# Kernel tuning notes

Measured on AMD Instinct MI355X. Metric: run time of the kernel, lower is better.

Reference implementation:

```python
import jax, jax.numpy as jnp
import numpy as np

N = 100000
E = 1600000
D_IN = 128
D_HID = 128
D_OUT = 128


def setup_inputs() -> dict:
    key = jax.random.key(0)
    ks = jax.random.split(key, 12)
    x = jax.random.normal(ks[0], (N, D_IN), dtype=jnp.float32)
    edge_index = jax.random.randint(ks[1], (2, E), 0, N, dtype=jnp.int32)
    def lin(k, fan_in, fan_out):
        s = 1.0 / np.sqrt(fan_in)
        return jax.random.uniform(k, (fan_in, fan_out), jnp.float32, -s, s)
    dims = [(D_IN, D_HID), (D_HID, D_HID), (D_HID, D_OUT)]
    inp = {"x": x, "edge_index": edge_index}
    for i, (fi, fo) in enumerate(dims):
        inp[f"Wl{i}"] = lin(ks[2 + 3 * i], fi, fo)
        inp[f"Wr{i}"] = lin(ks[3 + 3 * i], fi, fo)
        inp[f"b{i}"] = jnp.zeros((fo,), jnp.float32)
    return inp


def _sage_conv(h, row, col, Wl, Wr, b):
    # mean aggregation over incoming neighbors: out[i] = mean_{j->i} h[j]
    n = h.shape[0]
    agg = jax.ops.segment_sum(h[col], row, num_segments=n)  # [N, d]
    deg = jax.ops.segment_sum(jnp.ones_like(row, dtype=h.dtype), row, num_segments=n)
    agg = agg / jnp.maximum(deg, 1.0)[:, None]
    return agg @ Wl + b + h @ Wr


def reference(x, edge_index, Wl0, Wr0, b0, Wl1, Wr1, b1, Wl2, Wr2, b2):
    row, col = edge_index[0], edge_index[1]  # dst, src
    h1 = jax.nn.relu(_sage_conv(x, row, col, Wl0, Wr0, b0))   # dropout is no-op in eval
    h2 = jax.nn.relu(_sage_conv(h1, row, col, Wl1, Wr1, b1))
    h3 = jax.nn.relu(_sage_conv(h2, row, col, Wl2, Wr2, b2))
    return (h1, h2, h3)
```

## Files before the change

### kernel.cpp

```cpp
#include <hip/hip_runtime.h>

#define NN 100000
#define NE 1600000
#define DD 128
#define BM 64
#define NPB 256
#define NBUCK 391
#define ECHUNK 8192
#define NBLK_PART 196
#define CAP 8192
#define CVX_BLK 800
#define CVW_BLK 384

typedef __attribute__((ext_vector_type(4))) float f32x4;
typedef __attribute__((ext_vector_type(8))) short bf16x8;

__device__ inline unsigned short f2bf(float f) {
    unsigned int x = __builtin_bit_cast(unsigned int, f);
    unsigned int r = x + 0x7fffu + ((x >> 16) & 1u);
    return (unsigned short)(r >> 16);
}
__device__ inline float bf_lo(unsigned int u) { return __builtin_bit_cast(float, u << 16); }
__device__ inline float bf_hi(unsigned int u) { return __builtin_bit_cast(float, u & 0xffff0000u); }
__device__ inline unsigned int packbf(float a, float b) {
    return (unsigned int)f2bf(a) | ((unsigned int)f2bf(b) << 16);
}

__device__ inline void load_g2l_16(const void* gsrc, void* ldst) {
    __builtin_amdgcn_global_load_lds(
        (const __attribute__((address_space(1))) void*)(uintptr_t)gsrc,
        (__attribute__((address_space(3))) void*)(uintptr_t)ldst,
        16, 0, 0);
}


__global__ __launch_bounds__(256) void prep_kernel(
    const float* __restrict__ x, unsigned short* __restrict__ xb,
    const float* __restrict__ w0, const float* __restrict__ w1,
    const float* __restrict__ w2, const float* __restrict__ w3,
    const float* __restrict__ w4, const float* __restrict__ w5,
    unsigned short* __restrict__ wtall,
    const int* __restrict__ row, int* __restrict__ gcnt) {
    __shared__ int cnt[NBUCK];
    const int b = blockIdx.x;
    if (b < CVX_BLK) {
        int i = b * 256 + threadIdx.x;
        const int n4 = NN * DD / 4;
        for (; i < n4; i += CVX_BLK * 256) {
            float4 v = reinterpret_cast<const float4*>(x)[i];
            ushort4 o;
            o.x = f2bf(v.x); o.y = f2bf(v.y); o.z = f2bf(v.z); o.w = f2bf(v.w);
            reinterpret_cast<ushort4*>(xb)[i] = o;
        }
    } else if (b < CVX_BLK + CVW_BLK) {
        int t = (b - CVX_BLK) * 256 + threadIdx.x;
        int i = t >> 14;
        int r = t & 16383;
        const float* W = (i == 0) ? w0 : (i == 1) ? w1 : (i == 2) ? w2
                        : (i == 3) ? w3 : (i == 4) ? w4 : w5;
        int c = r >> 7, k = r & 127;
        wtall[t] = f2bf(W[k * DD + c]);
    } else {
        for (int i = threadIdx.x; i < NBUCK; i += 256) cnt[i] = 0;
        __syncthreads();
        int base = (b - CVX_BLK - CVW_BLK) * ECHUNK;
        int end = base + ECHUNK; if (end > NE) end = NE;
        for (int i = base + threadIdx.x; i < end; i += 256)
            atomicAdd(&cnt[row[i] >> 8], 1);
        __syncthreads();
        for (int i = threadIdx.x; i < NBUCK; i += 256) {
            int c = cnt[i];
            if (c) atomicAdd(&gcnt[i], c);
        }
    }
}


__global__ __launch_bounds__(512) void bucket_scan(const int* __restrict__ gcnt,
                                                   int* __restrict__ gbase) {
    __shared__ int sm[512];
    int t = threadIdx.x;
    sm[t] = (t < NBUCK) ? gcnt[t] : 0;
    __syncthreads();
    for (int off = 1; off < 512; off <<= 1) {
        int add = (t >= off) ? sm[t - off] : 0;
        __syncthreads();
        sm[t] += add;
        __syncthreads();
    }
    if (t < NBUCK) gbase[t + 1] = sm[t];
    if (t == 0) gbase[0] = 0;
}

__global__ __launch_bounds__(256) void bucket_scatter(const int* __restrict__ row,
                                                      const int* __restrict__ col,
                                                      const int* __restrict__ gbase,
                                                      int* __restrict__ gcursor,
                                                      uint2* __restrict__ ebuf) {
    __shared__ int cnt[NBUCK];
    __shared__ int base[NBUCK];
    for (int i = threadIdx.x; i < NBUCK; i += 256) cnt[i] = 0;
    __syncthreads();
    int cbase = blockIdx.x * ECHUNK;
    int cend = cbase + ECHUNK; if (cend > NE) cend = NE;
    for (int i = cbase + threadIdx.x; i < cend; i += 256)
        atomicAdd(&cnt[row[i] >> 8], 1);
    __syncthreads();
    for (int i = threadIdx.x; i < NBUCK; i += 256) {
        int c = cnt[i];
        cnt[i] = 0;
        base[i] = c ? (gbase[i] + atomicAdd(&gcursor[i], c)) : 0;
    }
    __syncthreads();
    for (int i = cbase + threadIdx.x; i < cend; i += 256) {
        int r = row[i], c = col[i];
        int b = r >> 8;
        int k = atomicAdd(&cnt[b], 1);
        ebuf[base[b] + k] = uint2{(unsigned)r, (unsigned)c};
    }
}

__global__ __launch_bounds__(256) void csr_build(const uint2* __restrict__ ebuf,
                                                 const int* __restrict__ gbase,
                                                 int* __restrict__ offs,
                                                 int* __restrict__ csr_col) {
    __shared__ int dcnt[NPB];
    __shared__ int doff[NPB];
    __shared__ int sm[NPB];
    __shared__ int stage[CAP];
    const int b = blockIdx.x;
    const int es = gbase[b], ee = gbase[b + 1];
    const int m = ee - es;
    const int t = threadIdx.x;
    const int nbase = b * NPB;

    dcnt[t] = 0;
    __syncthreads();
    for (int i = es + t; i < ee; i += 256) {
        int ln = (int)ebuf[i].x - nbase;
        atomicAdd(&dcnt[ln], 1);
    }
    __syncthreads();
    sm[t] = dcnt[t];
    __syncthreads();
    for (int off = 1; off < 256; off <<= 1) {
        int add = (t >= off) ? sm[t - off] : 0;
        __syncthreads();
        sm[t] += add;
        __syncthreads();
    }
    doff[t] = sm[t] - dcnt[t];
    int node = nbase + t;
    if (node < NN) offs[node + 1] = es + sm[t];
    if (b == 0 && t == 0) offs[0] = 0;
    dcnt[t] = 0;
    __syncthreads();

    if (m <= CAP) {
        for (int i = es + t; i < ee; i += 256) {
            uint2 e = ebuf[i];
            int ln = (int)e.x - nbase;
            int k = atomicAdd(&dcnt[ln], 1);
            stage[doff[ln] + k] = (int)e.y;
        }
        __syncthreads();
        for (int i = t; i < m; i += 256) csr_col[es + i] = stage[i];
    } else {
        for (int i = es + t; i < ee; i += 256) {
            uint2 e = ebuf[i];
            int ln = (int)e.x - nbase;
            int k = atomicAdd(&dcnt[ln], 1);
            csr_col[es + doff[ln] + k] = (int)e.y;
        }
    }
}


__global__ __launch_bounds__(256) void fused_layer(
    const unsigned short* __restrict__ hb,
    const int* __restrict__ offs, const int* __restrict__ csr_col,
    const unsigned short* __restrict__ WlT, const unsigned short* __restrict__ WrT,
    const float* __restrict__ bias, float* __restrict__ out,
    unsigned short* __restrict__ hbn) {
    __shared__ uint4 smem4[2048];
    char* AldsB = (char*)smem4;
    char* HldsB = AldsB + 16384;
    const int row0 = blockIdx.x * BM;
    const int tid = threadIdx.x;
    const int w = tid >> 6, l = tid & 63;

    const char* Hsrc = (const char*)(hb + (size_t)row0 * DD);
#pragma unroll
    for (int j = 0; j < 4; ++j) {
        int base = w * 4096 + j * 1024;
        int doff = base + l * 16;
        int soff = doff ^ (((doff >> 8) & 7) << 4);
        if (row0 + (doff >> 8) < NN) load_g2l_16(Hsrc + soff, HldsB + base);
    }

    const int g16 = tid >> 4, lane = tid & 15;
    for (int i = 0; i < 4; ++i) {
        const int rloc = g16 * 4 + i;
        const int node = row0 + rloc;
        float a0 = 0, a1 = 0, a2 = 0, a3 = 0, a4 = 0, a5 = 0, a6 = 0, a7 = 0;
        float inv = 0.0f;
        if (node < NN) {
            int s = offs[node], e = offs[node + 1];
            int p = s;
            for (; p + 8 <= e; p += 8) {
                uint4 v[8];
#pragma unroll
                for (int q = 0; q < 8; ++q) {
                    int c = csr_col[p + q];
                    v[q] = *reinterpret_cast<const uint4*>(hb + (size_t)c * DD + lane * 8);
                }
#pragma unroll
                for (int q = 0; q < 8; ++q) {
                    a0 += bf_lo(v[q].x); a1 += bf_hi(v[q].x);
                    a2 += bf_lo(v[q].y); a3 += bf_hi(v[q].y);
                    a4 += bf_lo(v[q].z); a5 += bf_hi(v[q].z);
                    a6 += bf_lo(v[q].w); a7 += bf_hi(v[q].w);
                }
            }
            for (; p < e; ++p) {
                int c = csr_col[p];
                uint4 v = *reinterpret_cast<const uint4*>(hb + (size_t)c * DD + lane * 8);
                a0 += bf_lo(v.x); a1 += bf_hi(v.x);
                a2 += bf_lo(v.y); a3 += bf_hi(v.y);
                a4 += bf_lo(v.z); a5 += bf_hi(v.z);
                a6 += bf_lo(v.w); a7 += bf_hi(v.w);
            }
            inv = (e > s) ? (1.0f / (float)(e - s)) : 0.0f;
        }
        uint4 o;
        o.x = packbf(a0 * inv, a1 * inv);
        o.y = packbf(a2 * inv, a3 * inv);
        o.z = packbf(a4 * inv, a5 * inv);
        o.w = packbf(a6 * inv, a7 * inv);
        int off = (rloc << 8) + ((lane * 16) ^ ((rloc & 7) << 4));
        *reinterpret_cast<uint4*>(AldsB + off) = o;
    }
    __syncthreads();

    const int wr = w & 1, wc = w >> 1;
    const int lrow = l & 15, lg = l >> 4;

    f32x4 acc[2][4];
#pragma unroll
    for (int m = 0; m < 2; ++m)
#pragma unroll
        for (int n = 0; n < 4; ++n) acc[m][n] = (f32x4){0.f, 0.f, 0.f, 0.f};

    float bv[4];
#pragma unroll
    for (int n = 0; n < 4; ++n) bv[n] = bias[wc * 64 + n * 16 + lrow];

#pragma unroll
    for (int kb = 0; kb < 4; ++kb) {
        const int kbyte = kb * 64 + lg * 16;
        bf16x8 aA[2], aH[2];
#pragma unroll
        for (int m = 0; m < 2; ++m) {
            int rloc = wr * 32 + m * 16 + lrow;
            int off = (rloc << 8) + kbyte;
            off ^= (rloc & 7) << 4;
            aA[m] = *reinterpret_cast<const bf16x8*>(AldsB + off);
            aH[m] = *reinterpret_cast<const bf16x8*>(HldsB + off);
        }
        bf16x8 bL[4], bR[4];
#pragma unroll
        for (int n = 0; n < 4; ++n) {
            size_t woff = ((size_t)(wc * 64 + n * 16 + lrow) << 7) + kb * 32 + lg * 8;
            bL[n] = *reinterpret_cast<const bf16x8*>(WlT + woff);
            bR[n] = *reinterpret_cast<const bf16x8*>(WrT + woff);
        }
#pragma unroll
        for (int m = 0; m < 2; ++m)
#pragma unroll
            for (int n = 0; n < 4; ++n) {
                acc[m][n] = __builtin_amdgcn_mfma_f32_16x16x32_bf16(aA[m], bL[n], acc[m][n], 0, 0, 0);
                acc[m][n] = __builtin_amdgcn_mfma_f32_16x16x32_bf16(aH[m], bR[n], acc[m][n], 0, 0, 0);
            }
    }

    __syncthreads();
    float* otile = (float*)smem4;
#pragma unroll
    for (int m = 0; m < 2; ++m) {
        int rb = wr * 32 + m * 16 + lg * 4;
#pragma unroll
        for (int n = 0; n < 4; ++n) {
            int c = wc * 64 + n * 16 + lrow;
#pragma unroll
            for (int j = 0; j < 4; ++j)
                otile[(rb + j) * DD + c] = fmaxf(acc[m][n][j] + bv[n], 0.0f);
        }
    }
    __syncthreads();
    const f32x4* t4 = (const f32x4*)smem4;
#pragma unroll
    for (int it = 0; it < 8; ++it) {
        int idx = it * 256 + tid;
        int r = idx >> 5;
        int gr = row0 + r;
        if (gr < NN) {
            f32x4 v = t4[idx];
            __builtin_nontemporal_store(v, (f32x4*)out + (size_t)gr * 32 + (idx & 31));
            if (hbn) {
                uint2 pk;
                pk.x = packbf(v[0], v[1]);
                pk.y = packbf(v[2], v[3]);
                *((uint2*)hbn + (size_t)gr * 32 + (idx & 31)) = pk;
            }
        }
    }
}

extern "C" void kernel_launch(void* const* d_in, const int* in_sizes, int n_in,
                              void* d_out, int out_size, void* d_ws, size_t ws_size,
                              hipStream_t stream) {
    const float* x = (const float*)d_in[0];
    const int* ei = (const int*)d_in[1];
    const int* row = ei;
    const int* col = ei + NE;
    const float* Wl[3] = {(const float*)d_in[2], (const float*)d_in[5], (const float*)d_in[8]};
    const float* Wr[3] = {(const float*)d_in[3], (const float*)d_in[6], (const float*)d_in[9]};
    const float* bb[3] = {(const float*)d_in[4], (const float*)d_in[7], (const float*)d_in[10]};
    float* out = (float*)d_out;

    char* ws = (char*)d_ws;
    auto carve = [&](size_t bytes) {
        char* p = ws;
        ws += (bytes + 255) & ~(size_t)255;
        return p;
    };
    unsigned short* buf0 = (unsigned short*)carve((size_t)NN * DD * 2);
    unsigned short* buf1 = (unsigned short*)carve((size_t)NN * DD * 2);
    unsigned short* wtall = (unsigned short*)carve((size_t)6 * DD * DD * 2);
    int* gcnt    = (int*)carve((size_t)2 * NBUCK * sizeof(int));
    int* gcursor = gcnt + NBUCK;
    int* gbase   = (int*)carve((size_t)(NBUCK + 1) * sizeof(int));
    int* offs    = (int*)carve((size_t)(NN + 1) * sizeof(int));
    uint2* ebuf  = (uint2*)carve((size_t)NE * sizeof(uint2));
    int* csr_col = (int*)carve((size_t)NE * sizeof(int));

    hipMemsetAsync(gcnt, 0, (size_t)2 * NBUCK * sizeof(int), stream);

    prep_kernel<<<CVX_BLK + CVW_BLK + NBLK_PART, 256, 0, stream>>>(
        x, buf0, Wl[0], Wr[0], Wl[1], Wr[1], Wl[2], Wr[2], wtall, row, gcnt);
    bucket_scan<<<1, 512, 0, stream>>>(gcnt, gbase);
    bucket_scatter<<<NBLK_PART, 256, 0, stream>>>(row, col, gbase, gcursor, ebuf);
    csr_build<<<NBUCK, 256, 0, stream>>>(ebuf, gbase, offs, csr_col);

    const int ngrid = (NN + BM - 1) / BM;

    unsigned short* hin = buf0;
    unsigned short* hout = buf1;
    for (int lyr = 0; lyr < 3; ++lyr) {
        float* o = out + (size_t)lyr * NN * DD;
        fused_layer<<<ngrid, 256, 0, stream>>>(
            hin, offs, csr_col,
            wtall + (size_t)2 * lyr * DD * DD, wtall + (size_t)(2 * lyr + 1) * DD * DD,
            bb[lyr], o, (lyr < 2) ? hout : (unsigned short*)nullptr);
        unsigned short* t = hin; hin = hout; hout = t;
    }
}
```

Before: 350.5 us.

## Split layer into feature-sliced gather kernel and separate GEMM kernel

Stores node features in eight 16-feature column slices (32 bytes per node per slice) so each aggregation block gathers from one 3.2MB slice that can stay resident in cache. The layer is split into an aggregation kernel, which uses dynamic row stealing via an LDS atomic counter and writes a sliced aggregate buffer, and a GEMM kernel that loads the sliced aggregate and self tiles with a new swizzle. The input conversion becomes its own kernel that writes the sliced layout. In exchange it adds an extra round trip of the aggregate buffer through global memory and an extra kernel launch per layer.

```diff
diff --git a/kernel.cpp b/kernel.cpp
--- a/kernel.cpp
+++ b/kernel.cpp
@@ -9,9 +9,12 @@
 #define ECHUNK 8192
 #define NBLK_PART 196
 #define CAP 8192
-#define CVX_BLK 800
 #define CVW_BLK 384
-
+#define SLICE_SHORTS ((size_t)NN * 16)
+#define AGG_TILE 1024
+#define AGG_GRID ((98) * 8)
+
+typedef __attribute__((ext_vector_type(2))) float f32x2;
 typedef __attribute__((ext_vector_type(4))) float f32x4;
 typedef __attribute__((ext_vector_type(8))) short bf16x8;
 
@@ -34,8 +37,7 @@
 }
 
 
-__global__ __launch_bounds__(256) void prep_kernel(
-    const float* __restrict__ x, unsigned short* __restrict__ xb,
+__global__ __launch_bounds__(256) void prep_wh(
     const float* __restrict__ w0, const float* __restrict__ w1,
     const float* __restrict__ w2, const float* __restrict__ w3,
     const float* __restrict__ w4, const float* __restrict__ w5,
@@ -43,17 +45,8 @@
     const int* __restrict__ row, int* __restrict__ gcnt) {
     __shared__ int cnt[NBUCK];
     const int b = blockIdx.x;
-    if (b < CVX_BLK) {
-        int i = b * 256 + threadIdx.x;
-        const int n4 = NN * DD / 4;
-        for (; i < n4; i += CVX_BLK * 256) {
-            float4 v = reinterpret_cast<const float4*>(x)[i];
-            ushort4 o;
-            o.x = f2bf(v.x); o.y = f2bf(v.y); o.z = f2bf(v.z); o.w = f2bf(v.w);
-            reinterpret_cast<ushort4*>(xb)[i] = o;
-        }
-    } else if (b < CVX_BLK + CVW_BLK) {
-        int t = (b - CVX_BLK) * 256 + threadIdx.x;
+    if (b < CVW_BLK) {
+        int t = b * 256 + threadIdx.x;
         int i = t >> 14;
         int r = t & 16383;
         const float* W = (i == 0) ? w0 : (i == 1) ? w1 : (i == 2) ? w2
@@ -63,7 +56,7 @@
     } else {
         for (int i = threadIdx.x; i < NBUCK; i += 256) cnt[i] = 0;
         __syncthreads();
-        int base = (b - CVX_BLK - CVW_BLK) * ECHUNK;
+        int base = (b - CVW_BLK) * ECHUNK;
         int end = base + ECHUNK; if (end > NE) end = NE;
         for (int i = base + threadIdx.x; i < end; i += 256)
             atomicAdd(&cnt[row[i] >> 8], 1);
@@ -71,6 +64,38 @@
         for (int i = threadIdx.x; i < NBUCK; i += 256) {
             int c = cnt[i];
             if (c) atomicAdd(&gcnt[i], c);
+        }
+    }
+}
+
+__global__ __launch_bounds__(256) void conv_x_sliced(const float* __restrict__ x,
+                                                     unsigned short* __restrict__ xs) {
+    __shared__ unsigned short tile[BM * DD];
+    const int row0 = blockIdx.x * BM;
+    const int tid = threadIdx.x;
+    char* ldsB = (char*)tile;
+#pragma unroll
+    for (int it = 0; it < 8; ++it) {
+        int idx = it * 256 + tid;
+        int r = idx >> 5, q4 = idx & 31;
+        if (row0 + r < NN) {
+            float4 v = *reinterpret_cast<const float4*>(&x[(size_t)(row0 + r) * DD + q4 * 4]);
+            uint2 pk;
+            pk.x = packbf(v.x, v.y);
+            pk.y = packbf(v.z, v.w);
+            *reinterpret_cast<uint2*>(ldsB + r * 256 + q4 * 8) = pk;
+        }
+    }
+    __syncthreads();
+#pragma unroll
+    for (int it = 0; it < 4; ++it) {
+        int u = it * 256 + tid;
+        int f = u >> 7, rem = u & 127;
+        int r = rem >> 1, half = rem & 1;
+        int n = row0 + r;
+        if (n < NN) {
+            uint4 v = *reinterpret_cast<const uint4*>(ldsB + r * 256 + f * 32 + half * 16);
+            *reinterpret_cast<uint4*>(xs + (size_t)f * SLICE_SHORTS + (size_t)n * 16 + half * 8) = v;
         }
     }
 }
@@ -176,69 +201,88 @@
 }
 
 
-__global__ __launch_bounds__(256) void fused_layer(
-    const unsigned short* __restrict__ hb,
-    const int* __restrict__ offs, const int* __restrict__ csr_col,
+__global__ __launch_bounds__(512) void agg_sliced(const unsigned short* __restrict__ hs,
+                                                  const int* __restrict__ offs,
+                                                  const int* __restrict__ csr_col,
+                                                  unsigned short* __restrict__ aggs) {
+    __shared__ int nextrow;
+    if (threadIdx.x == 0) nextrow = 0;
+    __syncthreads();
+    const int f = blockIdx.x & 7;
+    const int node0 = (blockIdx.x >> 3) * AGG_TILE;
+    const int lane = threadIdx.x & 63;
+    const int half = threadIdx.x & 1;
+    const unsigned short* hsf = hs + (size_t)f * SLICE_SHORTS + half * 8;
+    unsigned short* aggf = aggs + (size_t)f * SLICE_SHORTS + half * 8;
+
+    while (true) {
+        int r = 0;
+        if (!(lane & 1)) r = atomicAdd(&nextrow, 1);
+        r = __shfl(r, lane & ~1, 64);
+        if (r >= AGG_TILE) break;
+        int n = node0 + r;
+        if (n >= NN) continue;
+        int s = offs[n], e = offs[n + 1];
+        f32x2 a0 = {0.f, 0.f}, a1 = {0.f, 0.f}, a2 = {0.f, 0.f}, a3 = {0.f, 0.f};
+        int p = s;
+        for (; p + 8 <= e; p += 8) {
+            uint4 v[8];
+#pragma unroll
+            for (int q = 0; q < 8; ++q) {
+                int c = csr_col[p + q];
+                v[q] = *reinterpret_cast<const uint4*>(hsf + (size_t)c * 16);
+            }
+#pragma unroll
+            for (int q = 0; q < 8; ++q) {
+                a0 += (f32x2){bf_lo(v[q].x), bf_hi(v[q].x)};
+                a1 += (f32x2){bf_lo(v[q].y), bf_hi(v[q].y)};
+                a2 += (f32x2){bf_lo(v[q].z), bf_hi(v[q].z)};
+                a3 += (f32x2){bf_lo(v[q].w), bf_hi(v[q].w)};
+            }
+        }
+        for (; p < e; ++p) {
+            int c = csr_col[p];
+            uint4 v = *reinterpret_cast<const uint4*>(hsf + (size_t)c * 16);
+            a0 += (f32x2){bf_lo(v.x), bf_hi(v.x)};
+            a1 += (f32x2){bf_lo(v.y), bf_hi(v.y)};
+            a2 += (f32x2){bf_lo(v.z), bf_hi(v.z)};
+            a3 += (f32x2){bf_lo(v.w), bf_hi(v.w)};
+        }
+        float inv = (e > s) ? (1.0f / (float)(e - s)) : 0.0f;
+        uint4 o;
+        o.x = packbf(a0[0] * inv, a0[1] * inv);
+        o.y = packbf(a1[0] * inv, a1[1] * inv);
+        o.z = packbf(a2[0] * inv, a2[1] * inv);
+        o.w = packbf(a3[0] * inv, a3[1] * inv);
+        *reinterpret_cast<uint4*>(aggf + (size_t)n * 16) = o;
+    }
+}
+
+
+__global__ __launch_bounds__(256) void gemm_sliced(
+    const unsigned short* __restrict__ aggs, const unsigned short* __restrict__ hs,
     const unsigned short* __restrict__ WlT, const unsigned short* __restrict__ WrT,
     const float* __restrict__ bias, float* __restrict__ out,
     unsigned short* __restrict__ hbn) {
     __shared__ uint4 smem4[2048];
-    char* AldsB = (char*)smem4;
-    char* HldsB = AldsB + 16384;
+    char* ldsB = (char*)smem4;
     const int row0 = blockIdx.x * BM;
     const int tid = threadIdx.x;
     const int w = tid >> 6, l = tid & 63;
 
-    const char* Hsrc = (const char*)(hb + (size_t)row0 * DD);
-#pragma unroll
-    for (int j = 0; j < 4; ++j) {
-        int base = w * 4096 + j * 1024;
-        int doff = base + l * 16;
-        int soff = doff ^ (((doff >> 8) & 7) << 4);
-        if (row0 + (doff >> 8) < NN) load_g2l_16(Hsrc + soff, HldsB + base);
-    }
-
-    const int g16 = tid >> 4, lane = tid & 15;
-    for (int i = 0; i < 4; ++i) {
-        const int rloc = g16 * 4 + i;
-        const int node = row0 + rloc;
-        float a0 = 0, a1 = 0, a2 = 0, a3 = 0, a4 = 0, a5 = 0, a6 = 0, a7 = 0;
-        float inv = 0.0f;
-        if (node < NN) {
-            int s = offs[node], e = offs[node + 1];
-            int p = s;
-            for (; p + 8 <= e; p += 8) {
-                uint4 v[8];
-#pragma unroll
-                for (int q = 0; q < 8; ++q) {
-                    int c = csr_col[p + q];
-                    v[q] = *reinterpret_cast<const uint4*>(hb + (size_t)c * DD + lane * 8);
-                }
-#pragma unroll
-                for (int q = 0; q < 8; ++q) {
-                    a0 += bf_lo(v[q].x); a1 += bf_hi(v[q].x);
-                    a2 += bf_lo(v[q].y); a3 += bf_hi(v[q].y);
-                    a4 += bf_lo(v[q].z); a5 += bf_hi(v[q].z);
-                    a6 += bf_lo(v[q].w); a7 += bf_hi(v[q].w);
-                }
-            }
-            for (; p < e; ++p) {
-                int c = csr_col[p];
-                uint4 v = *reinterpret_cast<const uint4*>(hb + (size_t)c * DD + lane * 8);
-                a0 += bf_lo(v.x); a1 += bf_hi(v.x);
-                a2 += bf_lo(v.y); a3 += bf_hi(v.y);
-                a4 += bf_lo(v.z); a5 += bf_hi(v.z);
-                a6 += bf_lo(v.w); a7 += bf_hi(v.w);
-            }
-            inv = (e > s) ? (1.0f / (float)(e - s)) : 0.0f;
-        }
-        uint4 o;
-        o.x = packbf(a0 * inv, a1 * inv);
-        o.y = packbf(a2 * inv, a3 * inv);
-        o.z = packbf(a4 * inv, a5 * inv);
-        o.w = packbf(a6 * inv, a7 * inv);
-        int off = (rloc << 8) + ((lane * 16) ^ ((rloc & 7) << 4));
-        *reinterpret_cast<uint4*>(AldsB + off) = o;
+#pragma unroll
+    for (int j = 0; j < 8; ++j) {
+        int u = w * 8 + j;
+        int chunk = u >> 1, halfc = u & 1;
+        int tile = chunk >> 3, f = chunk & 7;
+        int pos = halfc * 1024 + l * 16;
+        int r = pos >> 5, sub = pos & 31;
+        int S = ((r >> 2) & 1) << 4;
+        const unsigned short* srcbase = (tile == 0 ? aggs : hs) + (size_t)f * SLICE_SHORTS;
+        if (row0 + r < NN) {
+            load_g2l_16(srcbase + (size_t)(row0 + r) * 16 + ((sub ^ S) >> 1),
+                        ldsB + tile * 16384 + f * 2048 + pos);
+        }
     }
     __syncthreads();
 
@@ -258,14 +302,14 @@
 #pragma unroll
     for (int kb = 0; kb < 4; ++kb) {
         const int kbyte = kb * 64 + lg * 16;
+        const int f = kbyte >> 5, sub = kbyte & 31;
         bf16x8 aA[2], aH[2];
 #pragma unroll
         for (int m = 0; m < 2; ++m) {
-            int rloc = wr * 32 + m * 16 + lrow;
-            int off = (rloc << 8) + kbyte;
-            off ^= (rloc & 7) << 4;
-            aA[m] = *reinterpret_cast<const bf16x8*>(AldsB + off);
-            aH[m] = *reinterpret_cast<const bf16x8*>(HldsB + off);
+            int r = wr * 32 + m * 16 + lrow;
+            int off = f * 2048 + r * 32 + (sub ^ (((r >> 2) & 1) << 4));
+            aA[m] = *reinterpret_cast<const bf16x8*>(ldsB + off);
+            aH[m] = *reinterpret_cast<const bf16x8*>(ldsB + 16384 + off);
         }
         bf16x8 bL[4], bR[4];
 #pragma unroll
@@ -303,14 +347,24 @@
         int idx = it * 256 + tid;
         int r = idx >> 5;
         int gr = row0 + r;
-        if (gr < NN) {
-            f32x4 v = t4[idx];
-            __builtin_nontemporal_store(v, (f32x4*)out + (size_t)gr * 32 + (idx & 31));
-            if (hbn) {
-                uint2 pk;
-                pk.x = packbf(v[0], v[1]);
-                pk.y = packbf(v[2], v[3]);
-                *((uint2*)hbn + (size_t)gr * 32 + (idx & 31)) = pk;
+        if (gr < NN)
+            __builtin_nontemporal_store(t4[idx], (f32x4*)out + (size_t)gr * 32 + (idx & 31));
+    }
+    if (hbn) {
+#pragma unroll
+        for (int it = 0; it < 4; ++it) {
+            int u = it * 256 + tid;
+            int f = u >> 7, rem = u & 127;
+            int r = rem >> 1, half = rem & 1;
+            int n = row0 + r;
+            if (n < NN) {
+                const float* src = otile + r * DD + f * 16 + half * 8;
+                uint4 pk;
+                pk.x = packbf(src[0], src[1]);
+                pk.y = packbf(src[2], src[3]);
+                pk.z = packbf(src[4], src[5]);
+                pk.w = packbf(src[6], src[7]);
+                *reinterpret_cast<uint4*>(hbn + (size_t)f * SLICE_SHORTS + (size_t)n * 16 + half * 8) = pk;
             }
         }
     }
@@ -336,6 +390,7 @@
     };
     unsigned short* buf0 = (unsigned short*)carve((size_t)NN * DD * 2);
     unsigned short* buf1 = (unsigned short*)carve((size_t)NN * DD * 2);
+    unsigned short* aggs = (unsigned short*)carve((size_t)NN * DD * 2);
     unsigned short* wtall = (unsigned short*)carve((size_t)6 * DD * DD * 2);
     int* gcnt    = (int*)carve((size_t)2 * NBUCK * sizeof(int));
     int* gcursor = gcnt + NBUCK;
@@ -346,21 +401,21 @@
 
     hipMemsetAsync(gcnt, 0, (size_t)2 * NBUCK * sizeof(int), stream);
 
-    prep_kernel<<<CVX_BLK + CVW_BLK + NBLK_PART, 256, 0, stream>>>(
-        x, buf0, Wl[0], Wr[0], Wl[1], Wr[1], Wl[2], Wr[2], wtall, row, gcnt);
+    const int ngrid = (NN + BM - 1) / BM;
+    conv_x_sliced<<<ngrid, 256, 0, stream>>>(x, buf0);
+    prep_wh<<<CVW_BLK + NBLK_PART, 256, 0, stream>>>(
+        Wl[0], Wr[0], Wl[1], Wr[1], Wl[2], Wr[2], wtall, row, gcnt);
     bucket_scan<<<1, 512, 0, stream>>>(gcnt, gbase);
     bucket_scatter<<<NBLK_PART, 256, 0, stream>>>(row, col, gbase, gcursor, ebuf);
     csr_build<<<NBUCK, 256, 0, stream>>>(ebuf, gbase, offs, csr_col);
-
-    const int ngrid = (NN + BM - 1) / BM;
 
     unsigned short* hin = buf0;
     unsigned short* hout = buf1;
     for (int lyr = 0; lyr < 3; ++lyr) {
         float* o = out + (size_t)lyr * NN * DD;
-        fused_layer<<<ngrid, 256, 0, stream>>>(
-            hin, offs, csr_col,
-            wtall + (size_t)2 * lyr * DD * DD, wtall + (size_t)(2 * lyr + 1) * DD * DD,
+        agg_sliced<<<AGG_GRID, 512, 0, stream>>>(hin, offs, csr_col, aggs);
+        gemm_sliced<<<ngrid, 256, 0, stream>>>(
+            aggs, hin, wtall + (size_t)2 * lyr * DD * DD, wtall + (size_t)(2 * lyr + 1) * DD * DD,
             bb[lyr], o, (lyr < 2) ? hout : (unsigned short*)nullptr);
         unsigned short* t = hin; hin = hout; hout = t;
     }
```

Measured after the change: 480.8 us. 1.37x slower.
